# Kernel tuning notes

Hardware: AMD Instinct MI355X
Metric: run time of the kernel (lower is better)

The kernel has to match this reference:

```python
import jax, jax.numpy as jnp
import numpy as np

N = 32768          # nodes
E = 524288         # edges (avg degree 16)
H = 128            # hidden_features
EF = 16            # edge_features
MF = 2 * H + EF + 1  # message_features for e3, relaxed=False (distance feat = 1)


def _mlp2(x, W1, b1, W2, b2):
    # Linear -> silu -> Linear -> silu (edge_mlp)
    return jax.nn.silu(jax.nn.silu(x @ W1 + b1) @ W2 + b2)


def setup_inputs() -> dict:
    key = jax.random.key(0)
    ks = jax.random.split(key, 20)

    def glorot(k, shape):
        fan_in, fan_out = shape[0], shape[1]
        lim = np.sqrt(6.0 / (fan_in + fan_out)).astype(np.float32)
        return jax.random.uniform(k, shape, jnp.float32, -lim, lim)

    inp = {
        'src': jax.random.randint(ks[0], (E,), 0, N),
        'dst': jax.random.randint(ks[1], (E,), 0, N),
        'h': jax.random.normal(ks[2], (N, H), jnp.float32),
        'coords': jax.random.normal(ks[3], (N, 3), jnp.float32),
        'a': jax.random.normal(ks[4], (E, EF), jnp.float32),
        # coord_mlp: MF -> H -> H -> 1 (last bias-free, xavier gain 0.001)
        'W_c1': glorot(ks[5], (MF, H)), 'b_c1': jnp.zeros((H,), jnp.float32),
        'W_c2': glorot(ks[6], (H, H)),  'b_c2': jnp.zeros((H,), jnp.float32),
        'W_c3': glorot(ks[7], (H, 1)) * 0.001,
        # edge_mlp: MF -> H -> H
        'W_e1': glorot(ks[8], (MF, H)), 'b_e1': jnp.zeros((H,), jnp.float32),
        'W_e2': glorot(ks[9], (H, H)),  'b_e2': jnp.zeros((H,), jnp.float32),
        # att_mlp: H -> 1
        'W_att': glorot(ks[10], (H, 1)), 'b_att': jnp.zeros((1,), jnp.float32),
        # node_mlp: 2H -> H -> H
        'W_n1': glorot(ks[11], (2 * H, H)), 'b_n1': jnp.zeros((H,), jnp.float32),
        'W_n2': glorot(ks[12], (H, H)),     'b_n2': jnp.zeros((H,), jnp.float32),
    }
    return inp


def reference(src, dst, h, coords, a,
              W_c1, b_c1, W_c2, b_c2, W_c3,
              W_e1, b_e1, W_e2, b_e2,
              W_att, b_att,
              W_n1, b_n1, W_n2, b_n2):
    # --- edge gather + distance features (equivariance='e3', relaxed=False) ---
    srcs_x = coords[src]                      # [E, 3]
    dsts_x = coords[dst]
    diffs = srcs_x - dsts_x                   # [E, 3]
    radials = jnp.sum(diffs * diffs, axis=-1, keepdims=True)  # [E, 1]

    f = jnp.concatenate([h[src], h[dst], radials, a], axis=-1)  # [E, MF]

    # --- coord messages ---
    c = jax.nn.silu(f @ W_c1 + b_c1)
    c = jax.nn.silu(c @ W_c2 + b_c2)
    scale = c @ W_c3                          # [E, 1]
    msg_x = scale * diffs / (jnp.sqrt(radials + 1e-05) + 1.0)   # [E, 3]

    # --- hidden messages with attention gating ---
    msg_h = _mlp2(f, W_e1, b_e1, W_e2, b_e2)  # [E, H]
    att = jax.nn.sigmoid(msg_h @ W_att + b_att)  # [E, 1]
    msg_h = att * msg_h

    # --- scatter-sum aggregation at destination nodes ---
    x_agg = jax.ops.segment_sum(msg_x, dst, num_segments=N)  # [N, 3]
    h_agg = jax.ops.segment_sum(msg_h, dst, num_segments=N)  # [N, H]

    coords_out = coords + x_agg
    nh = jax.nn.silu(jnp.concatenate([h, h_agg], axis=-1) @ W_n1 + b_n1) @ W_n2 + b_n2
    h_out = h + nh
    return (h_out, coords_out)
```

## Files before the change

### kernel.cpp

```cpp
#include <hip/hip_runtime.h>
#include <math.h>

#define HD   128
#define EFD  16
#define MT   64
#define LPA  264
#define LPC  136

#define W1SZ (128 * 288)
#define W2SZ (128 * 128)
#define O_WE1 (W1SZ)
#define O_WC2 (2 * W1SZ)
#define O_WE2 (2 * W1SZ + W2SZ)
#define O_WN1 (2 * W1SZ + 2 * W2SZ)
#define O_WN2 (2 * W1SZ + 2 * W2SZ + 128 * 256)
#define WS_ELEMS (O_WN2 + W2SZ)

#define B_PSC   ((size_t)0)
#define B_PDC   ((size_t)8388608)
#define B_PSE   ((size_t)16777216)
#define B_PDE   ((size_t)25165824)
#define B_WPAN  ((size_t)33554432)
#define B_CNT   ((size_t)33865728)
#define B_OFS   ((size_t)33996800)
#define B_SRCP  ((size_t)34127872)
#define B_DSTP  ((size_t)36225024)
#define B_EIDX  ((size_t)38322176)

typedef __attribute__((ext_vector_type(8))) short short8;
typedef __attribute__((ext_vector_type(4))) float f32x4;

__device__ __forceinline__ unsigned short f2bf(float x) {
    __bf16 b = (__bf16)x;
    unsigned short u;
    __builtin_memcpy(&u, &b, 2);
    return u;
}
__device__ __forceinline__ float bfl(unsigned u) {
    union { unsigned u; float f; } v; v.u = u << 16; return v.f;
}
__device__ __forceinline__ float bfh(unsigned u) {
    union { unsigned u; float f; } v; v.u = u & 0xffff0000u; return v.f;
}
__device__ __forceinline__ float sigm_f(float x) {
    return __builtin_amdgcn_rcpf(1.f + __expf(-x));
}
__device__ __forceinline__ float silu_f(float x) { return x * sigm_f(x); }
__device__ __forceinline__ unsigned pack2(float a, float b) {
    return (unsigned)f2bf(a) | ((unsigned)f2bf(b) << 16);
}

__device__ __forceinline__ void frag_l1(int idx, const float* __restrict__ W,
                                        const float* __restrict__ bias,
                                        unsigned short* __restrict__ out)
{
    const int j = idx & 7, lane = (idx >> 3) & 63, blk = idx >> 9;
    const int kc = blk % 9, n = blk / 9;
    const int k = kc * 32 + (lane >> 4) * 8 + j;
    const int c = n * 16 + (lane & 15);
    float v = 0.f;
    if (k < 256) v = W[k * HD + c];
    else if (k < 272) v = W[(k + 1) * HD + c];
    else if (k == 272) v = W[256 * HD + c];
    else if (k == 273) v = bias[c];
    out[idx] = f2bf(v);
}
__device__ __forceinline__ void frag_sq(int idx, const float* __restrict__ W,
                                        int nkc, unsigned short* __restrict__ out)
{
    const int j = idx & 7, lane = (idx >> 3) & 63, blk = idx >> 9;
    const int kc = blk % nkc, n = blk / nkc;
    const int k = kc * 32 + (lane >> 4) * 8 + j;
    const int c = n * 16 + (lane & 15);
    out[idx] = f2bf(W[k * HD + c]);
}

__global__ __launch_bounds__(256) void fused_prep(
    const float* __restrict__ Wc1, const float* __restrict__ bc1,
    const float* __restrict__ We1, const float* __restrict__ be1,
    const float* __restrict__ Wc2, const float* __restrict__ We2,
    const float* __restrict__ Wn1, const float* __restrict__ Wn2,
    unsigned short* __restrict__ ws,
    const int* __restrict__ dst, unsigned* __restrict__ cnt,
    int nPrep, int E)
{
    const int bid = blockIdx.x, tid = threadIdx.x;
    if (bid < nPrep) {
        int idx = bid * 256 + tid;
        if (idx < W1SZ)            { frag_l1(idx, Wc1, bc1, ws);            return; }
        idx -= W1SZ;
// ... 68 lines not shown

    #pragma unroll
    for (int it = 0; it < 8; ++it) {
        const int idx = it * 256 + tid;
        const int r = idx >> 5, q = idx & 31;
        const float4 v = *(const float4*)(h + (size_t)(n0 + r) * HD + q * 4);
        uint2 p; p.x = pack2(v.x, v.y); p.y = pack2(v.z, v.w);
        *(uint2*)&hsh[r][q * 4] = p;
    }
    __syncthreads();

    const int lane = tid & 63;
    const int w    = tid >> 6;
    const int w2   = w * 2;
    const int col  = lane & 15;
    const int kg   = lane >> 4;

    pre_pass(wpan + lane * 8,         &hsh[0][0], Psc, Pdc, n0, w2, w, col, kg);
    pre_pass(wpan + O_WE1 + lane * 8, &hsh[0][0], Pse, Pde, n0, w2, w, col, kg);
}

__global__ __launch_bounds__(1024) void scan32k(const unsigned* __restrict__ cnt,
                                                unsigned* __restrict__ ofs)
{
    __shared__ unsigned wsum[16];
    __shared__ unsigned carry_s;
    const int tid = threadIdx.x, lane = tid & 63, w = tid >> 6;
    if (tid == 0) carry_s = 0;
    __syncthreads();
    for (int c = 0; c < 32; ++c) {
        const unsigned x = cnt[c * 1024 + tid];
        unsigned v = x;
        #pragma unroll
        for (int off = 1; off < 64; off <<= 1) {
            unsigned t = __shfl_up(v, off);
            if (lane >= off) v += t;
        }
        if (lane == 63) wsum[w] = v;
        __syncthreads();
        if (tid < 16) {
            unsigned s = wsum[tid];
            #pragma unroll
            for (int off = 1; off < 16; off <<= 1) {
                unsigned t = __shfl_up(s, off);
                if (tid >= off) s += t;
            }
            wsum[tid] = s;
        }
        __syncthreads();
        const unsigned carry = carry_s;
        const unsigned woff = (w == 0) ? 0u : wsum[w - 1];
        ofs[c * 1024 + tid] = carry + woff + v - x;
        __syncthreads();
        if (tid == 0) carry_s = carry + wsum[15];
        __syncthreads();
    }
}

__global__ __launch_bounds__(256) void scatter_perm(
    const int* __restrict__ src, const int* __restrict__ dst,
    unsigned* __restrict__ ofs,
    int* __restrict__ srcp, int* __restrict__ dstp,
    int* __restrict__ eidx, int E)
{
    const int i = blockIdx.x * 256 + threadIdx.x;
    if (i >= E) return;
    const int d = dst[i];
    const unsigned pos = atomicAdd(&ofs[d], 1u);
    srcp[pos] = src[i];
    dstp[pos] = d;
    eidx[pos] = i;
}

__global__ __launch_bounds__(256, 4) void edge_kernel(
    const int* __restrict__ srcp, const int* __restrict__ dstp,
    const int* __restrict__ eidx, const float* __restrict__ a,
    const float* __restrict__ coords,
    const unsigned short* __restrict__ Psc, const unsigned short* __restrict__ Pdc,
    const unsigned short* __restrict__ Pse, const unsigned short* __restrict__ Pde,
    const float* __restrict__ bc2, const float* __restrict__ Wc3,
    const float* __restrict__ be2,
    const float* __restrict__ Watt, const float* __restrict__ batt,
    const unsigned short* __restrict__ wpan,
    float* __restrict__ out_h, float* __restrict__ out_x)
{
    __shared__ __align__(16) unsigned short csh_c[MT][LPC];
    __shared__ __align__(16) unsigned short csh_e[MT][LPC];
    __shared__ float diff_s[MT][3];
    __shared__ float rad_s[MT];
    __shared__ float rinv_s[MT];
    __shared__ float sc_part[4][MT];
    __shared__ float pa_part[4][MT];
    __shared__ float att_s[MT];
    __shared__ float sc_s[MT];
    __shared__ int   src_s[MT], dst_s[MT], eid_s[MT];
    __shared__ short run_start[MT + 1];
    __shared__ int   nruns_s;

    const int tid = threadIdx.x;
    const int e0  = blockIdx.x * MT;

    if (tid < MT) {
        const int s = srcp[e0 + tid], d = dstp[e0 + tid];
        src_s[tid] = s; dst_s[tid] = d;
        eid_s[tid] = eidx[e0 + tid];
        const float dx = coords[(size_t)s*3+0] - coords[(size_t)d*3+0];
        const float dy = coords[(size_t)s*3+1] - coords[(size_t)d*3+1];
        const float dz = coords[(size_t)s*3+2] - coords[(size_t)d*3+2];
        diff_s[tid][0] = dx; diff_s[tid][1] = dy; diff_s[tid][2] = dz;
        const float rad = dx*dx + dy*dy + dz*dz;
        rad_s[tid]  = rad;
        rinv_s[tid] = __builtin_amdgcn_rcpf(sqrtf(rad + 1e-5f) + 1.f);
    }
    __syncthreads();

    if (tid < 64) {
        const bool st = (tid == 0) || (dst_s[tid] != dst_s[tid - 1]);
        unsigned long long m = __ballot(st);
        if (tid == 0) {
            int nr = 0;
            while (m) { run_start[nr++] = (short)__builtin_ctzll(m); m &= m - 1; }
            run_start[nr] = MT;
            nruns_s = nr;
        }
    }

    const int lane = tid & 63;
    const int w    = tid >> 6;
    const int w2   = w * 2;
    const int col  = lane & 15;
    const int kg   = lane >> 4;

    const unsigned short* Wc1p = wpan            + lane * 8;
    const unsigned short* We1p = wpan + O_WE1    + lane * 8;
    const unsigned short* Wc2p = wpan + O_WC2    + lane * 8;
    const unsigned short* We2p = wpan + O_WE2    + lane * 8;

    short8 idf;
    #pragma unroll
    for (int j = 0; j < 8; ++j)
        idf[j] = (short)((((kg * 8 + j) & 15) == col) ? 0x3F80 : 0);

    const unsigned short* bas_c[4];
    const unsigned short* bas_e[4];
    #pragma unroll
    for (int et = 0; et < 4; ++et) {
        const int r = et * 16 + col;
        const size_t so = (size_t)src_s[r] * HD;
        const size_t dofs = (size_t)dst_s[r] * HD;
        const int slot = (kg & 1) * 8;
        bas_c[et] = ((kg < 2) ? Psc + so : Pdc + dofs) + slot;
        bas_e[et] = ((kg < 2) ? Pse + so : Pde + dofs) + slot;
    }

    const short8 zf = {0,0,0,0,0,0,0,0};
    const f32x4 zero = {0.f, 0.f, 0.f, 0.f};
    f32x4 ac[2][4], ae[2][4];

    #pragma unroll
    for (int m = 0; m < 2; ++m)
        #pragma unroll
        for (int et = 0; et < 4; ++et) { ac[m][et] = zero; ae[m][et] = zero; }

    #pragma unroll
    for (int m = 0; m < 2; ++m) {
        const int co = (w2 + m) * 16;
        #pragma unroll
        for (int et = 0; et < 4; ++et) {
            const short8 bc_ = *(const short8*)(bas_c[et] + co);
            const short8 be_ = *(const short8*)(bas_e[et] + co);
            ac[m][et] = __builtin_amdgcn_mfma_f32_16x16x32_bf16(idf, bc_, ac[m][et], 0, 0, 0);
            ae[m][et] = __builtin_amdgcn_mfma_f32_16x16x32_bf16(idf, be_, ae[m][et], 0, 0, 0);
        }
    }
    {
        short8 df[4];
        #pragma unroll
        for (int et = 0; et < 4; ++et) {
            if (kg < 2) {
                const int oe = eid_s[et * 16 + col];
                const float4 a0 = *(const float4*)(a + (size_t)oe * EFD + kg * 8);
                const float4 a1 = *(const float4*)(a + (size_t)oe * EFD + kg * 8 + 4);
                short8 v;
                v[0] = (short)f2bf(a0.x); v[1] = (short)f2bf(a0.y);
                v[2] = (short)f2bf(a0.z); v[3] = (short)f2bf(a0.w);
                v[4] = (short)f2bf(a1.x); v[5] = (short)f2bf(a1.y);
                v[6] = (short)f2bf(a1.z); v[7] = (short)f2bf(a1.w);
                df[et] = v;
            } else if (kg == 2) {
                short8 v = zf;
                v[0] = (short)f2bf(rad_s[et * 16 + col]);
                v[1] = (short)0x3F80;
                df[et] = v;
            } else df[et] = zf;
        }
        #pragma unroll
        for (int m = 0; m < 2; ++m) {
            const short8 wc = *(const short8*)&Wc1p[((w2 + m) * 9 + 8) << 9];
            const short8 we = *(const short8*)&We1p[((w2 + m) * 9 + 8) << 9];
            #pragma unroll
            for (int et = 0; et < 4; ++et) {
                ac[m][et] = __builtin_amdgcn_mfma_f32_16x16x32_bf16(wc, df[et], ac[m][et], 0, 0, 0);
                ae[m][et] = __builtin_amdgcn_mfma_f32_16x16x32_bf16(we, df[et], ae[m][et], 0, 0, 0);
            }
        }
    }
    #pragma unroll
    for (int m = 0; m < 2; ++m)
        #pragma unroll
        for (int et = 0; et < 4; ++et) {
            const int row = et * 16 + col;
            const int hw  = w * 32 + m * 16 + kg * 4;
            uint2 vc, ve;
            vc.x = pack2(silu_f(ac[m][et][0]), silu_f(ac[m][et][1]));
            vc.y = pack2(silu_f(ac[m][et][2]), silu_f(ac[m][et][3]));
            ve.x = pack2(silu_f(ae[m][et][0]), silu_f(ae[m][et][1]));
            ve.y = pack2(silu_f(ae[m][et][2]), silu_f(ae[m][et][3]));
            *(uint2*)&csh_c[row][hw] = vc;
            *(uint2*)&csh_e[row][hw] = ve;
        }
    __syncthreads();

    #pragma unroll
    for (int m = 0; m < 2; ++m)
        #pragma unroll
        for (int et = 0; et < 4; ++et) { ac[m][et] = zero; ae[m][et] = zero; }

    #pragma unroll
    for (int kc = 0; kc < 4; ++kc) {
        short8 dc[4], de[4];
        #pragma unroll
        for (int et = 0; et < 4; ++et) {
            const int row = et * 16 + col;
            dc[et] = *(const short8*)&csh_c[row][kc * 32 + kg * 8];
            de[et] = *(const short8*)&csh_e[row][kc * 32 + kg * 8];
        }
        #pragma unroll
        for (int m = 0; m < 2; ++m) {
            const short8 wc = *(const short8*)&Wc2p[((w2 + m) * 4 + kc) << 9];
            const short8 we = *(const short8*)&We2p[((w2 + m) * 4 + kc) << 9];
            #pragma unroll
            for (int et = 0; et < 4; ++et) {
                ac[m][et] = __builtin_amdgcn_mfma_f32_16x16x32_bf16(wc, dc[et], ac[m][et], 0, 0, 0);
                ae[m][et] = __builtin_amdgcn_mfma_f32_16x16x32_bf16(we, de[et], ae[m][et], 0, 0, 0);
            }
        }
    }

    {
        float sc[4] = {0.f, 0.f, 0.f, 0.f};
        #pragma unroll
        for (int m = 0; m < 2; ++m)
            #pragma unroll
            for (int i = 0; i < 4; ++i) {
                const int hw = w * 32 + m * 16 + kg * 4 + i;
                const float b = bc2[hw], w3 = Wc3[hw];
                #pragma unroll
                for (int et = 0; et < 4; ++et)
                    sc[et] += silu_f(ac[m][et][i] + b) * w3;
            }
        #pragma unroll
        for (int et = 0; et < 4; ++et) {
            sc[et] += __shfl_xor(sc[et], 16);
            sc[et] += __shfl_xor(sc[et], 32);
        }
        if (kg == 0) {
            #pragma unroll
            for (int et = 0; et < 4; ++et)
                sc_part[w][et * 16 + col] = sc[et];
        }
    }
    __syncthreads();

    {
        float pa[4] = {0.f, 0.f, 0.f, 0.f};
        #pragma unroll
        for (int m = 0; m < 2; ++m)
            #pragma unroll
            for (int et = 0; et < 4; ++et) {
                const int row = et * 16 + col;
                const int hw  = w * 32 + m * 16 + kg * 4;
                const float v0 = silu_f(ae[m][et][0] + be2[hw]);
                const float v1 = silu_f(ae[m][et][1] + be2[hw+1]);
                const float v2 = silu_f(ae[m][et][2] + be2[hw+2]);
                const float v3 = silu_f(ae[m][et][3] + be2[hw+3]);
                pa[et] += v0 * Watt[hw] + v1 * Watt[hw+1]
                        + v2 * Watt[hw+2] + v3 * Watt[hw+3];
                uint2 ve;
                ve.x = pack2(v0, v1);
                ve.y = pack2(v2, v3);
                *(uint2*)&csh_e[row][hw] = ve;
            }
        #pragma unroll
        for (int et = 0; et < 4; ++et) {
            pa[et] += __shfl_xor(pa[et], 16);
            pa[et] += __shfl_xor(pa[et], 32);
        }
        if (kg == 0) {
            #pragma unroll
            for (int et = 0; et < 4; ++et)
                pa_part[w][et * 16 + col] = pa[et];
        }
    }
    __syncthreads();

    if (tid < MT) {
        att_s[tid] = sigm_f(pa_part[0][tid] + pa_part[1][tid] +
                            pa_part[2][tid] + pa_part[3][tid] + batt[0]);
        sc_s[tid]  = (sc_part[0][tid] + sc_part[1][tid] +
                      sc_part[2][tid] + sc_part[3][tid]) * rinv_s[tid];
    }
    __syncthreads();

    {
        const int nr    = nruns_s;
        const int colx2 = tid & 63;
        for (int r = tid >> 6; r < nr; r += 4) {
            const int s0 = run_start[r], s1 = run_start[r + 1];
            float sum0 = 0.f, sum1 = 0.f;
            for (int e = s0; e < s1; ++e) {
                const unsigned uv = *(const unsigned*)&csh_e[e][colx2 * 2];
                const float at = att_s[e];
                sum0 += bfl(uv) * at;
                sum1 += bfh(uv) * at;
            }
            const int drow = dst_s[s0];
            float* op = out_h + (size_t)drow * HD + colx2 * 2;
            atomicAdd(op,     sum0);
            atomicAdd(op + 1, sum1);
            if (colx2 < 2) {
                float sx0 = 0.f, sx1 = 0.f;
                for (int e = s0; e < s1; ++e) {
                    const float s = sc_s[e];
                    sx0 += s * diff_s[e][colx2 * 2];
                    if (colx2 == 0) sx1 += s * diff_s[e][1];
                }
                atomicAdd(&out_x[(size_t)drow * 3 + colx2 * 2], sx0);
                if (colx2 == 0) atomicAdd(&out_x[(size_t)drow * 3 + 1], sx1);
            }
        }
    }
}

__global__ __launch_bounds__(256) void node_kernel(
    const float* __restrict__ h, const float* __restrict__ coords,
    const float* __restrict__ bn1, const float* __restrict__ bn2,
    const unsigned short* __restrict__ wpan,
    float* __restrict__ out_h, float* __restrict__ out_x)
{
    __shared__ __align__(16) unsigned short ash[MT][LPA];
    __shared__ __align__(16) unsigned short csh[MT][LPC];

    const int tid = threadIdx.x;
    const int n0  = blockIdx.x * MT;

    #pragma unroll
    for (int it = 0; it < 16; ++it) {
        const int idx = it * 256 + tid;
        const int e = idx >> 6, q = idx & 63;
        const float* base = (q < 32)
            ? h     + (size_t)(n0 + e) * HD + q * 4
            : out_h + (size_t)(n0 + e) * HD + (q - 32) * 4;
        const float4 v = *(const float4*)base;
        uint2 p; p.x = pack2(v.x, v.y); p.y = pack2(v.z, v.w);
        *(uint2*)&ash[e][q * 4] = p;
    }
    __syncthreads();

    if (tid < MT * 3) {
        const int n = tid / 3, d = tid % 3;
        const size_t gi = (size_t)(n0 + n) * 3 + d;
        out_x[gi] += coords[gi];
    }

    const int lane = tid & 63;
    const int w    = tid >> 6;
    const int er0  = w * 16;
    const int col  = lane & 15;
    const int kg   = lane >> 4;

    const unsigned short* Wn1p = wpan + O_WN1 + lane * 8;
    const unsigned short* Wn2p = wpan + O_WN2 + lane * 8;

    const f32x4 zero = {0.f, 0.f, 0.f, 0.f};
    f32x4 acc[8];

    #pragma unroll
    for (int n = 0; n < 8; ++n) acc[n] = zero;
    #pragma unroll
    for (int kc = 0; kc < 8; ++kc) {
        const short8 af = *(const short8*)&ash[er0 + col][kc * 32 + kg * 8];
        #pragma unroll
        for (int n = 0; n < 8; ++n) {
            const short8 bf = *(const short8*)&Wn1p[(n * 8 + kc) << 9];
            acc[n] = __builtin_amdgcn_mfma_f32_16x16x32_bf16(af, bf, acc[n], 0, 0, 0);
        }
    }
    #pragma unroll
    for (int n = 0; n < 8; ++n) {
        const float b = bn1[n*16 + col];
        #pragma unroll
        for (int i = 0; i < 4; ++i)
            csh[er0 + kg*4 + i][n*16 + col] = f2bf(silu_f(acc[n][i] + b));
    }
    __syncthreads();
    #pragma unroll
    for (int n = 0; n < 8; ++n) acc[n] = zero;
    #pragma unroll
    for (int kc = 0; kc < 4; ++kc) {
        const short8 af = *(const short8*)&csh[er0 + col][kc * 32 + kg * 8];
        #pragma unroll
        for (int n = 0; n < 8; ++n) {
            const short8 bf = *(const short8*)&Wn2p[(n * 4 + kc) << 9];
            acc[n] = __builtin_amdgcn_mfma_f32_16x16x32_bf16(af, bf, acc[n], 0, 0, 0);
        }
    }
    #pragma unroll
    for (int i = 0; i < 4; ++i) {
        const int node = n0 + er0 + kg*4 + i;
        const float* hr   = h     + (size_t)node * HD;
        float*       orow = out_h + (size_t)node * HD;
        #pragma unroll
        for (int n = 0; n < 8; ++n) {
            const int f = n*16 + col;
            orow[f] = hr[f] + acc[n][i] + bn2[f];
        }
    }
}

extern "C" void kernel_launch(void* const* d_in, const int* in_sizes, int n_in,
                              void* d_out, int out_size, void* d_ws, size_t ws_size,
                              hipStream_t stream)
{
    const int*   src    = (const int*)  d_in[0];
    const int*   dst    = (const int*)  d_in[1];
    const float* h      = (const float*)d_in[2];
    const float* coords = (const float*)d_in[3];
    const float* a      = (const float*)d_in[4];
    const float* Wc1    = (const float*)d_in[5];
    const float* bc1    = (const float*)d_in[6];
    const float* Wc2    = (const float*)d_in[7];
    const float* bc2    = (const float*)d_in[8];
    const float* Wc3    = (const float*)d_in[9];
    const float* We1    = (const float*)d_in[10];
    const float* be1    = (const float*)d_in[11];
    const float* We2    = (const float*)d_in[12];
    const float* be2    = (const float*)d_in[13];
    const float* Watt   = (const float*)d_in[14];
    const float* batt   = (const float*)d_in[15];
    const float* Wn1    = (const float*)d_in[16];
    const float* bn1    = (const float*)d_in[17];
    const float* Wn2    = (const float*)d_in[18];
    const float* bn2    = (const float*)d_in[19];

    const int E = in_sizes[0];
    const int N = in_sizes[2] / HD;

    float* out_h = (float*)d_out;
    float* out_x = out_h + (size_t)N * HD;

    char* wsb = (char*)d_ws;
    unsigned short* Psc  = (unsigned short*)(wsb + B_PSC);
    unsigned short* Pdc  = (unsigned short*)(wsb + B_PDC);
    unsigned short* Pse  = (unsigned short*)(wsb + B_PSE);
    unsigned short* Pde  = (unsigned short*)(wsb + B_PDE);
    unsigned short* wpan = (unsigned short*)(wsb + B_WPAN);
    unsigned*       cnt  = (unsigned*)      (wsb + B_CNT);
    unsigned*       ofs  = (unsigned*)      (wsb + B_OFS);
    int*            srcp = (int*)           (wsb + B_SRCP);
    int*            dstp = (int*)           (wsb + B_DSTP);
    int*            eidx = (int*)           (wsb + B_EIDX);

    hipMemsetAsync(d_out, 0, (size_t)out_size * sizeof(float), stream);
    hipMemsetAsync(cnt, 0, (size_t)N * sizeof(unsigned), stream);

    const int nPrep = WS_ELEMS / 256;
    const int nHist = (E + 255) / 256;

    fused_prep<<<dim3(nPrep + nHist), dim3(256), 0, stream>>>(
        Wc1, bc1, We1, be1, Wc2, We2, Wn1, Wn2, wpan,
        dst, cnt, nPrep, E);

    node_pre<<<dim3(N / MT), dim3(256), 0, stream>>>(
        h, wpan, Psc, Pdc, Pse, Pde);

    scan32k<<<dim3(1), dim3(1024), 0, stream>>>(cnt, ofs);
    scatter_perm<<<dim3((E + 255) / 256), dim3(256), 0, stream>>>(
        src, dst, ofs, srcp, dstp, eidx, E);

    edge_kernel<<<dim3(E / MT), dim3(256), 0, stream>>>(
        srcp, dstp, eidx, a, coords,
        Psc, Pdc, Pse, Pde,
        bc2, Wc3, be2, Watt, batt,
        wpan, out_h, out_x);

    node_kernel<<<dim3(N / MT), dim3(256), 0, stream>>>(
        h, coords, bn1, bn2, wpan, out_h, out_x);
}
```

Before: 312.0 us.

## Make edge kernel persistent with software-prefetched gathers for the next tile

The edge kernel now launches 1024 blocks that each loop over several 64-edge tiles instead of one block per tile. Index loads, the precomputed-projection gathers, edge-id loads and coordinate reads for the next tile are issued into registers and double-buffered shared arrays while the current tile finishes its MLP and scatter. The goal is to hide gather latency behind compute and cut per-block launch and setup cost. In exchange the kernel holds more live registers, which can lower occupancy, and runs fewer blocks.

```diff
diff --git a/kernel.cpp b/kernel.cpp
--- a/kernel.cpp
+++ b/kernel.cpp
@@ -240,7 +240,7 @@
     const float* __restrict__ be2,
     const float* __restrict__ Watt, const float* __restrict__ batt,
     const unsigned short* __restrict__ wpan,
-    float* __restrict__ out_h, float* __restrict__ out_x)
+    float* __restrict__ out_h, float* __restrict__ out_x, int ntPer)
 {
     __shared__ __align__(16) unsigned short csh_c[MT][LPC];
     __shared__ __align__(16) unsigned short csh_e[MT][LPC];
@@ -251,43 +251,17 @@
     __shared__ float pa_part[4][MT];
     __shared__ float att_s[MT];
     __shared__ float sc_s[MT];
-    __shared__ int   src_s[MT], dst_s[MT], eid_s[MT];
-    __shared__ short run_start[MT + 1];
+    __shared__ int   src_s[2][MT], dst_s[2][MT];
+    __shared__ short run_start[MT + 2];
     __shared__ int   nruns_s;
 
-    const int tid = threadIdx.x;
-    const int e0  = blockIdx.x * MT;
-
-    if (tid < MT) {
-        const int s = srcp[e0 + tid], d = dstp[e0 + tid];
-        src_s[tid] = s; dst_s[tid] = d;
-        eid_s[tid] = eidx[e0 + tid];
-        const float dx = coords[(size_t)s*3+0] - coords[(size_t)d*3+0];
-        const float dy = coords[(size_t)s*3+1] - coords[(size_t)d*3+1];
-        const float dz = coords[(size_t)s*3+2] - coords[(size_t)d*3+2];
-        diff_s[tid][0] = dx; diff_s[tid][1] = dy; diff_s[tid][2] = dz;
-        const float rad = dx*dx + dy*dy + dz*dz;
-        rad_s[tid]  = rad;
-        rinv_s[tid] = __builtin_amdgcn_rcpf(sqrtf(rad + 1e-5f) + 1.f);
-    }
-    __syncthreads();
-
-    if (tid < 64) {
-        const bool st = (tid == 0) || (dst_s[tid] != dst_s[tid - 1]);
-        unsigned long long m = __ballot(st);
-        if (tid == 0) {
-            int nr = 0;
-            while (m) { run_start[nr++] = (short)__builtin_ctzll(m); m &= m - 1; }
-            run_start[nr] = MT;
-            nruns_s = nr;
-        }
-    }
-
+    const int tid  = threadIdx.x;
     const int lane = tid & 63;
     const int w    = tid >> 6;
     const int w2   = w * 2;
     const int col  = lane & 15;
     const int kg   = lane >> 4;
+    const int tile0 = blockIdx.x * ntPer;
 
     const unsigned short* Wc1p = wpan            + lane * 8;
     const unsigned short* We1p = wpan + O_WE1    + lane * 8;
@@ -299,202 +273,258 @@
     for (int j = 0; j < 8; ++j)
         idf[j] = (short)((((kg * 8 + j) & 15) == col) ? 0x3F80 : 0);
 
-    const unsigned short* bas_c[4];
-    const unsigned short* bas_e[4];
-    #pragma unroll
-    for (int et = 0; et < 4; ++et) {
-        const int r = et * 16 + col;
-        const size_t so = (size_t)src_s[r] * HD;
-        const size_t dofs = (size_t)dst_s[r] * HD;
-        const int slot = (kg & 1) * 8;
-        bas_c[et] = ((kg < 2) ? Psc + so : Pdc + dofs) + slot;
-        bas_e[et] = ((kg < 2) ? Pse + so : Pde + dofs) + slot;
-    }
-
     const short8 zf = {0,0,0,0,0,0,0,0};
     const f32x4 zero = {0.f, 0.f, 0.f, 0.f};
-    f32x4 ac[2][4], ae[2][4];
-
-    #pragma unroll
-    for (int m = 0; m < 2; ++m)
-        #pragma unroll
-        for (int et = 0; et < 4; ++et) { ac[m][et] = zero; ae[m][et] = zero; }
-
-    #pragma unroll
-    for (int m = 0; m < 2; ++m) {
-        const int co = (w2 + m) * 16;
+
+    short8 pfc[2][4], pfe[2][4];
+    int    eidn[4];
+    float  cxs[3], cxd[3];
+
+    auto issue_gathers = [&](int buf, int e1) {
         #pragma unroll
         for (int et = 0; et < 4; ++et) {
-            const short8 bc_ = *(const short8*)(bas_c[et] + co);
-            const short8 be_ = *(const short8*)(bas_e[et] + co);
-            ac[m][et] = __builtin_amdgcn_mfma_f32_16x16x32_bf16(idf, bc_, ac[m][et], 0, 0, 0);
-            ae[m][et] = __builtin_amdgcn_mfma_f32_16x16x32_bf16(idf, be_, ae[m][et], 0, 0, 0);
-        }
-    }
+            const int r = et * 16 + col;
+            const size_t so   = (size_t)src_s[buf][r] * HD;
+            const size_t dofs = (size_t)dst_s[buf][r] * HD;
+            const int slot = (kg & 1) * 8;
+            const unsigned short* bc = ((kg < 2) ? Psc + so : Pdc + dofs) + slot;
+            const unsigned short* be = ((kg < 2) ? Pse + so : Pde + dofs) + slot;
+            pfc[0][et] = *(const short8*)(bc + w2 * 16);
+            pfc[1][et] = *(const short8*)(bc + (w2 + 1) * 16);
+            pfe[0][et] = *(const short8*)(be + w2 * 16);
+            pfe[1][et] = *(const short8*)(be + (w2 + 1) * 16);
+            eidn[et] = eidx[e1 + r];
+        }
+    };
+    auto issue_coords = [&](int buf) {
+        if (tid < MT) {
+            const int s = src_s[buf][tid], d = dst_s[buf][tid];
+            cxs[0] = coords[(size_t)s*3+0]; cxs[1] = coords[(size_t)s*3+1]; cxs[2] = coords[(size_t)s*3+2];
+            cxd[0] = coords[(size_t)d*3+0]; cxd[1] = coords[(size_t)d*3+1]; cxd[2] = coords[(size_t)d*3+2];
+        }
+    };
+
     {
-        short8 df[4];
-        #pragma unroll
-        for (int et = 0; et < 4; ++et) {
-            if (kg < 2) {
-                const int oe = eid_s[et * 16 + col];
-                const float4 a0 = *(const float4*)(a + (size_t)oe * EFD + kg * 8);
-                const float4 a1 = *(const float4*)(a + (size_t)oe * EFD + kg * 8 + 4);
-                short8 v;
-                v[0] = (short)f2bf(a0.x); v[1] = (short)f2bf(a0.y);
-                v[2] = (short)f2bf(a0.z); v[3] = (short)f2bf(a0.w);
-                v[4] = (short)f2bf(a1.x); v[5] = (short)f2bf(a1.y);
-                v[6] = (short)f2bf(a1.z); v[7] = (short)f2bf(a1.w);
-                df[et] = v;
-            } else if (kg == 2) {
-                short8 v = zf;
-                v[0] = (short)f2bf(rad_s[et * 16 + col]);
-                v[1] = (short)0x3F80;
-                df[et] = v;
-            } else df[et] = zf;
-        }
-        #pragma unroll
-        for (int m = 0; m < 2; ++m) {
-            const short8 wc = *(const short8*)&Wc1p[((w2 + m) * 9 + 8) << 9];
-            const short8 we = *(const short8*)&We1p[((w2 + m) * 9 + 8) << 9];
+        const int e1 = tile0 * MT;
+        if (tid < MT) {
+            src_s[0][tid] = srcp[e1 + tid];
+            dst_s[0][tid] = dstp[e1 + tid];
+        }
+        __syncthreads();
+        issue_gathers(0, e1);
+        issue_coords(0);
+    }
+
+    for (int t = 0; t < ntPer; ++t) {
+        const int cur = t & 1, nxt = cur ^ 1;
+        const int e0  = (tile0 + t) * MT;
+        const bool more = (t + 1 < ntPer);
+
+        __syncthreads();
+
+        if (tid < MT) {
+            const float dx = cxs[0] - cxd[0];
+            const float dy = cxs[1] - cxd[1];
+            const float dz = cxs[2] - cxd[2];
+            diff_s[tid][0] = dx; diff_s[tid][1] = dy; diff_s[tid][2] = dz;
+            const float rad = dx*dx + dy*dy + dz*dz;
+            rad_s[tid]  = rad;
+            rinv_s[tid] = __builtin_amdgcn_rcpf(sqrtf(rad + 1e-5f) + 1.f);
+            const bool st = (tid == 0) || (dst_s[cur][tid] != dst_s[cur][tid - 1]);
+            unsigned long long m = __ballot(st);
+            if (tid == 0) {
+                int nr = 0;
+                while (m) { run_start[nr++] = (short)__builtin_ctzll(m); m &= m - 1; }
+                run_start[nr] = MT;
+                nruns_s = nr;
+            }
+        }
+        __syncthreads();
+
+        f32x4 ac[2][4], ae[2][4];
+
+        #pragma unroll
+        for (int m = 0; m < 2; ++m)
             #pragma unroll
             for (int et = 0; et < 4; ++et) {
-                ac[m][et] = __builtin_amdgcn_mfma_f32_16x16x32_bf16(wc, df[et], ac[m][et], 0, 0, 0);
-                ae[m][et] = __builtin_amdgcn_mfma_f32_16x16x32_bf16(we, df[et], ae[m][et], 0, 0, 0);
-            }
-        }
-    }
-    #pragma unroll
-    for (int m = 0; m < 2; ++m)
-        #pragma unroll
-        for (int et = 0; et < 4; ++et) {
-            const int row = et * 16 + col;
-            const int hw  = w * 32 + m * 16 + kg * 4;
-            uint2 vc, ve;
-            vc.x = pack2(silu_f(ac[m][et][0]), silu_f(ac[m][et][1]));
-            vc.y = pack2(silu_f(ac[m][et][2]), silu_f(ac[m][et][3]));
-            ve.x = pack2(silu_f(ae[m][et][0]), silu_f(ae[m][et][1]));
-            ve.y = pack2(silu_f(ae[m][et][2]), silu_f(ae[m][et][3]));
-            *(uint2*)&csh_c[row][hw] = vc;
-            *(uint2*)&csh_e[row][hw] = ve;
-        }
-    __syncthreads();
-
-    #pragma unroll
-    for (int m = 0; m < 2; ++m)
-        #pragma unroll
-        for (int et = 0; et < 4; ++et) { ac[m][et] = zero; ae[m][et] = zero; }
-
-    #pragma unroll
-    for (int kc = 0; kc < 4; ++kc) {
-        short8 dc[4], de[4];
-        #pragma unroll
-        for (int et = 0; et < 4; ++et) {
-            const int row = et * 16 + col;
-            dc[et] = *(const short8*)&csh_c[row][kc * 32 + kg * 8];
-            de[et] = *(const short8*)&csh_e[row][kc * 32 + kg * 8];
-        }
-        #pragma unroll
-        for (int m = 0; m < 2; ++m) {
-            const short8 wc = *(const short8*)&Wc2p[((w2 + m) * 4 + kc) << 9];
-            const short8 we = *(const short8*)&We2p[((w2 + m) * 4 + kc) << 9];
+                ac[m][et] = __builtin_amdgcn_mfma_f32_16x16x32_bf16(idf, pfc[m][et], zero, 0, 0, 0);
+                ae[m][et] = __builtin_amdgcn_mfma_f32_16x16x32_bf16(idf, pfe[m][et], zero, 0, 0, 0);
+            }
+        {
+            short8 df[4];
             #pragma unroll
             for (int et = 0; et < 4; ++et) {
-                ac[m][et] = __builtin_amdgcn_mfma_f32_16x16x32_bf16(wc, dc[et], ac[m][et], 0, 0, 0);
-                ae[m][et] = __builtin_amdgcn_mfma_f32_16x16x32_bf16(we, de[et], ae[m][et], 0, 0, 0);
-            }
-        }
-    }
-
-    {
-        float sc[4] = {0.f, 0.f, 0.f, 0.f};
-        #pragma unroll
-        for (int m = 0; m < 2; ++m)
-            #pragma unroll
-            for (int i = 0; i < 4; ++i) {
-                const int hw = w * 32 + m * 16 + kg * 4 + i;
-                const float b = bc2[hw], w3 = Wc3[hw];
+                if (kg < 2) {
+                    const int oe = eidn[et];
+                    const float4 a0 = *(const float4*)(a + (size_t)oe * EFD + kg * 8);
+                    const float4 a1 = *(const float4*)(a + (size_t)oe * EFD + kg * 8 + 4);
+                    short8 v;
+                    v[0] = (short)f2bf(a0.x); v[1] = (short)f2bf(a0.y);
+                    v[2] = (short)f2bf(a0.z); v[3] = (short)f2bf(a0.w);
+                    v[4] = (short)f2bf(a1.x); v[5] = (short)f2bf(a1.y);
+                    v[6] = (short)f2bf(a1.z); v[7] = (short)f2bf(a1.w);
+                    df[et] = v;
+                } else if (kg == 2) {
+                    short8 v = zf;
+                    v[0] = (short)f2bf(rad_s[et * 16 + col]);
+                    v[1] = (short)0x3F80;
+                    df[et] = v;
+                } else df[et] = zf;
+            }
+            #pragma unroll
+            for (int m = 0; m < 2; ++m) {
+                const short8 wc = *(const short8*)&Wc1p[((w2 + m) * 9 + 8) << 9];
+                const short8 we = *(const short8*)&We1p[((w2 + m) * 9 + 8) << 9];
                 #pragma unroll
-                for (int et = 0; et < 4; ++et)
-                    sc[et] += silu_f(ac[m][et][i] + b) * w3;
-            }
-        #pragma unroll
-        for (int et = 0; et < 4; ++et) {
-            sc[et] += __shfl_xor(sc[et], 16);
-            sc[et] += __shfl_xor(sc[et], 32);
-        }
-        if (kg == 0) {
-            #pragma unroll
-            for (int et = 0; et < 4; ++et)
-                sc_part[w][et * 16 + col] = sc[et];
-        }
-    }
-    __syncthreads();
-
-    {
-        float pa[4] = {0.f, 0.f, 0.f, 0.f};
+                for (int et = 0; et < 4; ++et) {
+                    ac[m][et] = __builtin_amdgcn_mfma_f32_16x16x32_bf16(wc, df[et], ac[m][et], 0, 0, 0);
+                    ae[m][et] = __builtin_amdgcn_mfma_f32_16x16x32_bf16(we, df[et], ae[m][et], 0, 0, 0);
+                }
+            }
+        }
         #pragma unroll
         for (int m = 0; m < 2; ++m)
             #pragma unroll
             for (int et = 0; et < 4; ++et) {
                 const int row = et * 16 + col;
                 const int hw  = w * 32 + m * 16 + kg * 4;
-                const float v0 = silu_f(ae[m][et][0] + be2[hw]);
-                const float v1 = silu_f(ae[m][et][1] + be2[hw+1]);
-                const float v2 = silu_f(ae[m][et][2] + be2[hw+2]);
-                const float v3 = silu_f(ae[m][et][3] + be2[hw+3]);
-                pa[et] += v0 * Watt[hw] + v1 * Watt[hw+1]
-                        + v2 * Watt[hw+2] + v3 * Watt[hw+3];
-                uint2 ve;
-                ve.x = pack2(v0, v1);
-                ve.y = pack2(v2, v3);
+                uint2 vc, ve;
+                vc.x = pack2(silu_f(ac[m][et][0]), silu_f(ac[m][et][1]));
+                vc.y = pack2(silu_f(ac[m][et][2]), silu_f(ac[m][et][3]));
+                ve.x = pack2(silu_f(ae[m][et][0]), silu_f(ae[m][et][1]));
+                ve.y = pack2(silu_f(ae[m][et][2]), silu_f(ae[m][et][3]));
+                *(uint2*)&csh_c[row][hw] = vc;
                 *(uint2*)&csh_e[row][hw] = ve;
             }
-        #pragma unroll
-        for (int et = 0; et < 4; ++et) {
-            pa[et] += __shfl_xor(pa[et], 16);
-            pa[et] += __shfl_xor(pa[et], 32);
-        }
-        if (kg == 0) {
-            #pragma unroll
-            for (int et = 0; et < 4; ++et)
-                pa_part[w][et * 16 + col] = pa[et];
-        }
-    }
-    __syncthreads();
-
-    if (tid < MT) {
-        att_s[tid] = sigm_f(pa_part[0][tid] + pa_part[1][tid] +
-                            pa_part[2][tid] + pa_part[3][tid] + batt[0]);
-        sc_s[tid]  = (sc_part[0][tid] + sc_part[1][tid] +
-                      sc_part[2][tid] + sc_part[3][tid]) * rinv_s[tid];
-    }
-    __syncthreads();
-
-    {
-        const int nr    = nruns_s;
-        const int colx2 = tid & 63;
-        for (int r = tid >> 6; r < nr; r += 4) {
-            const int s0 = run_start[r], s1 = run_start[r + 1];
-            float sum0 = 0.f, sum1 = 0.f;
-            for (int e = s0; e < s1; ++e) {
-                const unsigned uv = *(const unsigned*)&csh_e[e][colx2 * 2];
-                const float at = att_s[e];
-                sum0 += bfl(uv) * at;
-                sum1 += bfh(uv) * at;
-            }
-            const int drow = dst_s[s0];
-            float* op = out_h + (size_t)drow * HD + colx2 * 2;
-            atomicAdd(op,     sum0);
-            atomicAdd(op + 1, sum1);
-            if (colx2 < 2) {
-                float sx0 = 0.f, sx1 = 0.f;
+        if (more && tid < MT) {
+            const int e1 = e0 + MT;
+            src_s[nxt][tid] = srcp[e1 + tid];
+            dst_s[nxt][tid] = dstp[e1 + tid];
+        }
+        __syncthreads();
+
+        #pragma unroll
+        for (int m = 0; m < 2; ++m)
+            #pragma unroll
+            for (int et = 0; et < 4; ++et) { ac[m][et] = zero; ae[m][et] = zero; }
+
+        #pragma unroll
+        for (int kc = 0; kc < 4; ++kc) {
+            short8 dc[4], de[4];
+            #pragma unroll
+            for (int et = 0; et < 4; ++et) {
+                const int row = et * 16 + col;
+                dc[et] = *(const short8*)&csh_c[row][kc * 32 + kg * 8];
+                de[et] = *(const short8*)&csh_e[row][kc * 32 + kg * 8];
+            }
+            #pragma unroll
+            for (int m = 0; m < 2; ++m) {
+                const short8 wc = *(const short8*)&Wc2p[((w2 + m) * 4 + kc) << 9];
+                const short8 we = *(const short8*)&We2p[((w2 + m) * 4 + kc) << 9];
+                #pragma unroll
+                for (int et = 0; et < 4; ++et) {
+                    ac[m][et] = __builtin_amdgcn_mfma_f32_16x16x32_bf16(wc, dc[et], ac[m][et], 0, 0, 0);
+                    ae[m][et] = __builtin_amdgcn_mfma_f32_16x16x32_bf16(we, de[et], ae[m][et], 0, 0, 0);
+                }
+            }
+        }
+
+        {
+            float sc[4] = {0.f, 0.f, 0.f, 0.f};
+            #pragma unroll
+            for (int m = 0; m < 2; ++m)
+                #pragma unroll
+                for (int i = 0; i < 4; ++i) {
+                    const int hw = w * 32 + m * 16 + kg * 4 + i;
+                    const float b = bc2[hw], w3 = Wc3[hw];
+                    #pragma unroll
+                    for (int et = 0; et < 4; ++et)
+                        sc[et] += silu_f(ac[m][et][i] + b) * w3;
+                }
+            #pragma unroll
+            for (int et = 0; et < 4; ++et) {
+                sc[et] += __shfl_xor(sc[et], 16);
+                sc[et] += __shfl_xor(sc[et], 32);
+            }
+            if (kg == 0) {
+                #pragma unroll
+                for (int et = 0; et < 4; ++et)
+                    sc_part[w][et * 16 + col] = sc[et];
+            }
+        }
+        __syncthreads();
+
+        {
+            float pa[4] = {0.f, 0.f, 0.f, 0.f};
+            #pragma unroll
+            for (int m = 0; m < 2; ++m)
+                #pragma unroll
+                for (int et = 0; et < 4; ++et) {
+                    const int row = et * 16 + col;
+                    const int hw  = w * 32 + m * 16 + kg * 4;
+                    const float v0 = silu_f(ae[m][et][0] + be2[hw]);
+                    const float v1 = silu_f(ae[m][et][1] + be2[hw+1]);
+                    const float v2 = silu_f(ae[m][et][2] + be2[hw+2]);
+                    const float v3 = silu_f(ae[m][et][3] + be2[hw+3]);
+                    pa[et] += v0 * Watt[hw] + v1 * Watt[hw+1]
+                            + v2 * Watt[hw+2] + v3 * Watt[hw+3];
+                    uint2 ve;
+                    ve.x = pack2(v0, v1);
+                    ve.y = pack2(v2, v3);
+                    *(uint2*)&csh_e[row][hw] = ve;
+                }
+            #pragma unroll
+            for (int et = 0; et < 4; ++et) {
+                pa[et] += __shfl_xor(pa[et], 16);
+                pa[et] += __shfl_xor(pa[et], 32);
+            }
+            if (kg == 0) {
+                #pragma unroll
+                for (int et = 0; et < 4; ++et)
+                    pa_part[w][et * 16 + col] = pa[et];
+            }
+        }
+        __syncthreads();
+
+        if (tid < MT) {
+            att_s[tid] = sigm_f(pa_part[0][tid] + pa_part[1][tid] +
+                                pa_part[2][tid] + pa_part[3][tid] + batt[0]);
+            sc_s[tid]  = (sc_part[0][tid] + sc_part[1][tid] +
+                          sc_part[2][tid] + sc_part[3][tid]) * rinv_s[tid];
+        }
+
+        if (more) {
+            issue_gathers(nxt, e0 + MT);
+            issue_coords(nxt);
+        }
+        __syncthreads();
+
+        {
+            const int nr    = nruns_s;
+            const int colx2 = tid & 63;
+            for (int r = tid >> 6; r < nr; r += 4) {
+                const int s0 = run_start[r], s1 = run_start[r + 1];
+                float sum0 = 0.f, sum1 = 0.f;
                 for (int e = s0; e < s1; ++e) {
-                    const float s = sc_s[e];
-                    sx0 += s * diff_s[e][colx2 * 2];
-                    if (colx2 == 0) sx1 += s * diff_s[e][1];
+                    const unsigned uv = *(const unsigned*)&csh_e[e][colx2 * 2];
+                    const float at = att_s[e];
+                    sum0 += bfl(uv) * at;
+                    sum1 += bfh(uv) * at;
                 }
-                atomicAdd(&out_x[(size_t)drow * 3 + colx2 * 2], sx0);
-                if (colx2 == 0) atomicAdd(&out_x[(size_t)drow * 3 + 1], sx1);
+                const int drow = dst_s[cur][s0];
+                float* op = out_h + (size_t)drow * HD + colx2 * 2;
+                atomicAdd(op,     sum0);
+                atomicAdd(op + 1, sum1);
+                if (colx2 < 2) {
+                    float sx0 = 0.f, sx1 = 0.f;
+                    for (int e = s0; e < s1; ++e) {
+                        const float s = sc_s[e];
+                        sx0 += s * diff_s[e][colx2 * 2];
+                        if (colx2 == 0) sx1 += s * diff_s[e][1];
+                    }
+                    atomicAdd(&out_x[(size_t)drow * 3 + colx2 * 2], sx0);
+                    if (colx2 == 0) atomicAdd(&out_x[(size_t)drow * 3 + 1], sx1);
+                }
             }
         }
     }
@@ -646,11 +676,15 @@
     scatter_perm<<<dim3((E + 255) / 256), dim3(256), 0, stream>>>(
         src, dst, ofs, srcp, dstp, eidx, E);
 
-    edge_kernel<<<dim3(E / MT), dim3(256), 0, stream>>>(
+    const int ntiles = E / MT;
+    int nblk = 1024, ntPer = ntiles / 1024;
+    if (ntiles % 1024) { nblk = ntiles; ntPer = 1; }
+
+    edge_kernel<<<dim3(nblk), dim3(256), 0, stream>>>(
         srcp, dstp, eidx, a, coords,
         Psc, Pdc, Pse, Pde,
         bc2, Wc3, be2, Watt, batt,
-        wpan, out_h, out_x);
+        wpan, out_h, out_x, ntPer);
 
     node_kernel<<<dim3(N / MT), dim3(256), 0, stream>>>(
         h, coords, bn1, bn2, wpan, out_h, out_x);
```

Result: slower. 766.6 us (+145.7%).

## Make edge kernel wave-independent with per-wave 16-edge tiles and no block barriers

Applied to the files above, without the earlier changes.

Restructures the edge kernel so each wave handles its own 16 edges end to end instead of four waves cooperating on a 64-edge tile split by output columns. Shared-memory staging, partial-sum tables and __syncthreads are replaced by per-wave LDS slices, wave barriers and shuffles for edge metadata, attention and scale values. This removes block-wide synchronisation and cross-wave reductions. In exchange, segment runs are shorter, so more atomics are issued per destination, and each wave now reads all of the layer weights itself.

```diff
diff --git a/kernel.cpp b/kernel.cpp
--- a/kernel.cpp
+++ b/kernel.cpp
@@ -4,8 +4,10 @@
 #define HD   128
 #define EFD  16
 #define MT   64
+#define WT   16
 #define LPA  264
 #define LPC  136
+#define LPW  132
 
 #define W1SZ (128 * 288)
 #define W2SZ (128 * 128)
@@ -242,52 +244,42 @@
     const unsigned short* __restrict__ wpan,
     float* __restrict__ out_h, float* __restrict__ out_x)
 {
-    __shared__ __align__(16) unsigned short csh_c[MT][LPC];
-    __shared__ __align__(16) unsigned short csh_e[MT][LPC];
-    __shared__ float diff_s[MT][3];
-    __shared__ float rad_s[MT];
-    __shared__ float rinv_s[MT];
-    __shared__ float sc_part[4][MT];
-    __shared__ float pa_part[4][MT];
-    __shared__ float att_s[MT];
-    __shared__ float sc_s[MT];
-    __shared__ int   src_s[MT], dst_s[MT], eid_s[MT];
-    __shared__ short run_start[MT + 1];
-    __shared__ int   nruns_s;
-
-    const int tid = threadIdx.x;
-    const int e0  = blockIdx.x * MT;
-
-    if (tid < MT) {
-        const int s = srcp[e0 + tid], d = dstp[e0 + tid];
-        src_s[tid] = s; dst_s[tid] = d;
-        eid_s[tid] = eidx[e0 + tid];
-        const float dx = coords[(size_t)s*3+0] - coords[(size_t)d*3+0];
-        const float dy = coords[(size_t)s*3+1] - coords[(size_t)d*3+1];
-        const float dz = coords[(size_t)s*3+2] - coords[(size_t)d*3+2];
-        diff_s[tid][0] = dx; diff_s[tid][1] = dy; diff_s[tid][2] = dz;
-        const float rad = dx*dx + dy*dy + dz*dz;
-        rad_s[tid]  = rad;
-        rinv_s[tid] = __builtin_amdgcn_rcpf(sqrtf(rad + 1e-5f) + 1.f);
-    }
-    __syncthreads();
-
-    if (tid < 64) {
-        const bool st = (tid == 0) || (dst_s[tid] != dst_s[tid - 1]);
-        unsigned long long m = __ballot(st);
-        if (tid == 0) {
-            int nr = 0;
-            while (m) { run_start[nr++] = (short)__builtin_ctzll(m); m &= m - 1; }
-            run_start[nr] = MT;
-            nruns_s = nr;
-        }
-    }
-
+    __shared__ __align__(16) unsigned short csh_c[4][WT][LPW];
+    __shared__ __align__(16) unsigned short csh_e[4][WT][LPW];
+
+    const int tid  = threadIdx.x;
     const int lane = tid & 63;
     const int w    = tid >> 6;
-    const int w2   = w * 2;
     const int col  = lane & 15;
     const int kg   = lane >> 4;
+    const int e0   = (blockIdx.x * 4 + w) * WT;
+
+    int srcv = 0, dstv = 0, eidv = 0;
+    float dfx = 0.f, dfy = 0.f, dfz = 0.f, radv = 0.f, rinvv = 0.f;
+    if (lane < WT) {
+        srcv = srcp[e0 + lane];
+        dstv = dstp[e0 + lane];
+        eidv = eidx[e0 + lane];
+        const float sx = coords[(size_t)srcv*3+0], sy = coords[(size_t)srcv*3+1], sz = coords[(size_t)srcv*3+2];
+        const float dx_ = coords[(size_t)dstv*3+0], dy_ = coords[(size_t)dstv*3+1], dz_ = coords[(size_t)dstv*3+2];
+        dfx = sx - dx_; dfy = sy - dy_; dfz = sz - dz_;
+        radv = dfx*dfx + dfy*dfy + dfz*dfz;
+        rinvv = __builtin_amdgcn_rcpf(sqrtf(radv + 1e-5f) + 1.f);
+    }
+    const int   se    = __shfl(srcv, col);
+    const int   de_   = __shfl(dstv, col);
+    const int   ee    = __shfl(eidv, col);
+    const float rad_c = __shfl(radv, col);
+
+    const int prevd = __shfl_up(dstv, 1);
+    const bool st = (lane < WT) && (lane == 0 || dstv != prevd);
+    const unsigned long long mask = __ballot(st) & 0xffffull;
+
+    const size_t so   = (size_t)se  * HD;
+    const size_t dofs = (size_t)de_ * HD;
+    const int slot = (kg & 1) * 8;
+    const unsigned short* bas_c = ((kg < 2) ? Psc + so : Pdc + dofs) + slot;
+    const unsigned short* bas_e = ((kg < 2) ? Pse + so : Pde + dofs) + slot;
 
     const unsigned short* Wc1p = wpan            + lane * 8;
     const unsigned short* We1p = wpan + O_WE1    + lane * 8;
@@ -299,202 +291,118 @@
     for (int j = 0; j < 8; ++j)
         idf[j] = (short)((((kg * 8 + j) & 15) == col) ? 0x3F80 : 0);
 
-    const unsigned short* bas_c[4];
-    const unsigned short* bas_e[4];
-    #pragma unroll
-    for (int et = 0; et < 4; ++et) {
-        const int r = et * 16 + col;
-        const size_t so = (size_t)src_s[r] * HD;
-        const size_t dofs = (size_t)dst_s[r] * HD;
-        const int slot = (kg & 1) * 8;
-        bas_c[et] = ((kg < 2) ? Psc + so : Pdc + dofs) + slot;
-        bas_e[et] = ((kg < 2) ? Pse + so : Pde + dofs) + slot;
-    }
-
     const short8 zf = {0,0,0,0,0,0,0,0};
     const f32x4 zero = {0.f, 0.f, 0.f, 0.f};
-    f32x4 ac[2][4], ae[2][4];
-
-    #pragma unroll
-    for (int m = 0; m < 2; ++m)
-        #pragma unroll
-        for (int et = 0; et < 4; ++et) { ac[m][et] = zero; ae[m][et] = zero; }
-
-    #pragma unroll
-    for (int m = 0; m < 2; ++m) {
-        const int co = (w2 + m) * 16;
-        #pragma unroll
-        for (int et = 0; et < 4; ++et) {
-            const short8 bc_ = *(const short8*)(bas_c[et] + co);
-            const short8 be_ = *(const short8*)(bas_e[et] + co);
-            ac[m][et] = __builtin_amdgcn_mfma_f32_16x16x32_bf16(idf, bc_, ac[m][et], 0, 0, 0);
-            ae[m][et] = __builtin_amdgcn_mfma_f32_16x16x32_bf16(idf, be_, ae[m][et], 0, 0, 0);
-        }
-    }
+
+    short8 df;
+    if (kg < 2) {
+        const float4 a0 = *(const float4*)(a + (size_t)ee * EFD + kg * 8);
+        const float4 a1 = *(const float4*)(a + (size_t)ee * EFD + kg * 8 + 4);
+        df[0] = (short)f2bf(a0.x); df[1] = (short)f2bf(a0.y);
+        df[2] = (short)f2bf(a0.z); df[3] = (short)f2bf(a0.w);
+        df[4] = (short)f2bf(a1.x); df[5] = (short)f2bf(a1.y);
+        df[6] = (short)f2bf(a1.z); df[7] = (short)f2bf(a1.w);
+    } else if (kg == 2) {
+        df = zf;
+        df[0] = (short)f2bf(rad_c);
+        df[1] = (short)0x3F80;
+    } else df = zf;
+
+    #pragma unroll
+    for (int m = 0; m < 8; ++m) {
+        const short8 bc_ = *(const short8*)(bas_c + m * 16);
+        const short8 be_ = *(const short8*)(bas_e + m * 16);
+        f32x4 ac = __builtin_amdgcn_mfma_f32_16x16x32_bf16(idf, bc_, zero, 0, 0, 0);
+        f32x4 ae = __builtin_amdgcn_mfma_f32_16x16x32_bf16(idf, be_, zero, 0, 0, 0);
+        const short8 wc = *(const short8*)&Wc1p[(m * 9 + 8) << 9];
+        const short8 we = *(const short8*)&We1p[(m * 9 + 8) << 9];
+        ac = __builtin_amdgcn_mfma_f32_16x16x32_bf16(wc, df, ac, 0, 0, 0);
+        ae = __builtin_amdgcn_mfma_f32_16x16x32_bf16(we, df, ae, 0, 0, 0);
+        const int hw = m * 16 + kg * 4;
+        uint2 vc, ve;
+        vc.x = pack2(silu_f(ac[0]), silu_f(ac[1]));
+        vc.y = pack2(silu_f(ac[2]), silu_f(ac[3]));
+        ve.x = pack2(silu_f(ae[0]), silu_f(ae[1]));
+        ve.y = pack2(silu_f(ae[2]), silu_f(ae[3]));
+        *(uint2*)&csh_c[w][col][hw] = vc;
+        *(uint2*)&csh_e[w][col][hw] = ve;
+    }
+    __builtin_amdgcn_wave_barrier();
+
+    short8 dc[4], de2[4];
+    #pragma unroll
+    for (int kc = 0; kc < 4; ++kc) {
+        dc[kc]  = *(const short8*)&csh_c[w][col][kc * 32 + kg * 8];
+        de2[kc] = *(const short8*)&csh_e[w][col][kc * 32 + kg * 8];
+    }
+    __builtin_amdgcn_wave_barrier();
+
+    float scl = 0.f, pal = 0.f;
+    #pragma unroll
+    for (int m = 0; m < 8; ++m) {
+        f32x4 ac = zero, ae = zero;
+        #pragma unroll
+        for (int kc = 0; kc < 4; ++kc) {
+            const short8 wc = *(const short8*)&Wc2p[(m * 4 + kc) << 9];
+            const short8 we = *(const short8*)&We2p[(m * 4 + kc) << 9];
+            ac = __builtin_amdgcn_mfma_f32_16x16x32_bf16(wc, dc[kc],  ac, 0, 0, 0);
+            ae = __builtin_amdgcn_mfma_f32_16x16x32_bf16(we, de2[kc], ae, 0, 0, 0);
+        }
+        const int hw = m * 16 + kg * 4;
+        const float4 b2 = *(const float4*)(bc2 + hw);
+        const float4 w3 = *(const float4*)(Wc3 + hw);
+        scl += silu_f(ac[0] + b2.x) * w3.x + silu_f(ac[1] + b2.y) * w3.y
+             + silu_f(ac[2] + b2.z) * w3.z + silu_f(ac[3] + b2.w) * w3.w;
+        const float4 be_ = *(const float4*)(be2 + hw);
+        const float4 wa  = *(const float4*)(Watt + hw);
+        const float v0 = silu_f(ae[0] + be_.x);
+        const float v1 = silu_f(ae[1] + be_.y);
+        const float v2 = silu_f(ae[2] + be_.z);
+        const float v3 = silu_f(ae[3] + be_.w);
+        pal += v0 * wa.x + v1 * wa.y + v2 * wa.z + v3 * wa.w;
+        uint2 ve;
+        ve.x = pack2(v0, v1);
+        ve.y = pack2(v2, v3);
+        *(uint2*)&csh_e[w][col][hw] = ve;
+    }
+    __builtin_amdgcn_wave_barrier();
+
+    scl += __shfl_xor(scl, 16);
+    scl += __shfl_xor(scl, 32);
+    pal += __shfl_xor(pal, 16);
+    pal += __shfl_xor(pal, 32);
+    const float att_v = sigm_f(pal + batt[0]);
+    const float sc_v  = scl * __shfl(rinvv, col);
+
     {
-        short8 df[4];
-        #pragma unroll
-        for (int et = 0; et < 4; ++et) {
-            if (kg < 2) {
-                const int oe = eid_s[et * 16 + col];
-                const float4 a0 = *(const float4*)(a + (size_t)oe * EFD + kg * 8);
-                const float4 a1 = *(const float4*)(a + (size_t)oe * EFD + kg * 8 + 4);
-                short8 v;
-                v[0] = (short)f2bf(a0.x); v[1] = (short)f2bf(a0.y);
-                v[2] = (short)f2bf(a0.z); v[3] = (short)f2bf(a0.w);
-                v[4] = (short)f2bf(a1.x); v[5] = (short)f2bf(a1.y);
-                v[6] = (short)f2bf(a1.z); v[7] = (short)f2bf(a1.w);
-                df[et] = v;
-            } else if (kg == 2) {
-                short8 v = zf;
-                v[0] = (short)f2bf(rad_s[et * 16 + col]);
-                v[1] = (short)0x3F80;
-                df[et] = v;
-            } else df[et] = zf;
-        }
-        #pragma unroll
-        for (int m = 0; m < 2; ++m) {
-            const short8 wc = *(const short8*)&Wc1p[((w2 + m) * 9 + 8) << 9];
-            const short8 we = *(const short8*)&We1p[((w2 + m) * 9 + 8) << 9];
-            #pragma unroll
-            for (int et = 0; et < 4; ++et) {
-                ac[m][et] = __builtin_amdgcn_mfma_f32_16x16x32_bf16(wc, df[et], ac[m][et], 0, 0, 0);
-                ae[m][et] = __builtin_amdgcn_mfma_f32_16x16x32_bf16(we, df[et], ae[m][et], 0, 0, 0);
-            }
-        }
-    }
-    #pragma unroll
-    for (int m = 0; m < 2; ++m)
-        #pragma unroll
-        for (int et = 0; et < 4; ++et) {
-            const int row = et * 16 + col;
-            const int hw  = w * 32 + m * 16 + kg * 4;
-            uint2 vc, ve;
-            vc.x = pack2(silu_f(ac[m][et][0]), silu_f(ac[m][et][1]));
-            vc.y = pack2(silu_f(ac[m][et][2]), silu_f(ac[m][et][3]));
-            ve.x = pack2(silu_f(ae[m][et][0]), silu_f(ae[m][et][1]));
-            ve.y = pack2(silu_f(ae[m][et][2]), silu_f(ae[m][et][3]));
-            *(uint2*)&csh_c[row][hw] = vc;
-            *(uint2*)&csh_e[row][hw] = ve;
-        }
-    __syncthreads();
-
-    #pragma unroll
-    for (int m = 0; m < 2; ++m)
-        #pragma unroll
-        for (int et = 0; et < 4; ++et) { ac[m][et] = zero; ae[m][et] = zero; }
-
-    #pragma unroll
-    for (int kc = 0; kc < 4; ++kc) {
-        short8 dc[4], de[4];
-        #pragma unroll
-        for (int et = 0; et < 4; ++et) {
-            const int row = et * 16 + col;
-            dc[et] = *(const short8*)&csh_c[row][kc * 32 + kg * 8];
-            de[et] = *(const short8*)&csh_e[row][kc * 32 + kg * 8];
-        }
-        #pragma unroll
-        for (int m = 0; m < 2; ++m) {
-            const short8 wc = *(const short8*)&Wc2p[((w2 + m) * 4 + kc) << 9];
-            const short8 we = *(const short8*)&We2p[((w2 + m) * 4 + kc) << 9];
-            #pragma unroll
-            for (int et = 0; et < 4; ++et) {
-                ac[m][et] = __builtin_amdgcn_mfma_f32_16x16x32_bf16(wc, dc[et], ac[m][et], 0, 0, 0);
-                ae[m][et] = __builtin_amdgcn_mfma_f32_16x16x32_bf16(we, de[et], ae[m][et], 0, 0, 0);
-            }
-        }
-    }
-
-    {
-        float sc[4] = {0.f, 0.f, 0.f, 0.f};
-        #pragma unroll
-        for (int m = 0; m < 2; ++m)
-            #pragma unroll
-            for (int i = 0; i < 4; ++i) {
-                const int hw = w * 32 + m * 16 + kg * 4 + i;
-                const float b = bc2[hw], w3 = Wc3[hw];
-                #pragma unroll
-                for (int et = 0; et < 4; ++et)
-                    sc[et] += silu_f(ac[m][et][i] + b) * w3;
-            }
-        #pragma unroll
-        for (int et = 0; et < 4; ++et) {
-            sc[et] += __shfl_xor(sc[et], 16);
-            sc[et] += __shfl_xor(sc[et], 32);
-        }
-        if (kg == 0) {
-            #pragma unroll
-            for (int et = 0; et < 4; ++et)
-                sc_part[w][et * 16 + col] = sc[et];
-        }
-    }
-    __syncthreads();
-
-    {
-        float pa[4] = {0.f, 0.f, 0.f, 0.f};
-        #pragma unroll
-        for (int m = 0; m < 2; ++m)
-            #pragma unroll
-            for (int et = 0; et < 4; ++et) {
-                const int row = et * 16 + col;
-                const int hw  = w * 32 + m * 16 + kg * 4;
-                const float v0 = silu_f(ae[m][et][0] + be2[hw]);
-                const float v1 = silu_f(ae[m][et][1] + be2[hw+1]);
-                const float v2 = silu_f(ae[m][et][2] + be2[hw+2]);
-                const float v3 = silu_f(ae[m][et][3] + be2[hw+3]);
-                pa[et] += v0 * Watt[hw] + v1 * Watt[hw+1]
-                        + v2 * Watt[hw+2] + v3 * Watt[hw+3];
-                uint2 ve;
-                ve.x = pack2(v0, v1);
-                ve.y = pack2(v2, v3);
-                *(uint2*)&csh_e[row][hw] = ve;
-            }
-        #pragma unroll
-        for (int et = 0; et < 4; ++et) {
-            pa[et] += __shfl_xor(pa[et], 16);
-            pa[et] += __shfl_xor(pa[et], 32);
-        }
-        if (kg == 0) {
-            #pragma unroll
-            for (int et = 0; et < 4; ++et)
-                pa_part[w][et * 16 + col] = pa[et];
-        }
-    }
-    __syncthreads();
-
-    if (tid < MT) {
-        att_s[tid] = sigm_f(pa_part[0][tid] + pa_part[1][tid] +
-                            pa_part[2][tid] + pa_part[3][tid] + batt[0]);
-        sc_s[tid]  = (sc_part[0][tid] + sc_part[1][tid] +
-                      sc_part[2][tid] + sc_part[3][tid]) * rinv_s[tid];
-    }
-    __syncthreads();
-
-    {
-        const int nr    = nruns_s;
-        const int colx2 = tid & 63;
-        for (int r = tid >> 6; r < nr; r += 4) {
-            const int s0 = run_start[r], s1 = run_start[r + 1];
-            float sum0 = 0.f, sum1 = 0.f;
+        unsigned long long mm = mask;
+        while (mm) {
+            const int s0 = (int)__builtin_ctzll(mm);
+            mm &= mm - 1;
+            const int s1 = mm ? (int)__builtin_ctzll(mm) : WT;
+            float sum0 = 0.f, sum1 = 0.f, sx0 = 0.f, sx1 = 0.f;
             for (int e = s0; e < s1; ++e) {
-                const unsigned uv = *(const unsigned*)&csh_e[e][colx2 * 2];
-                const float at = att_s[e];
+                const unsigned uv = *(const unsigned*)&csh_e[w][e][lane * 2];
+                const float at = __shfl(att_v, e);
                 sum0 += bfl(uv) * at;
                 sum1 += bfh(uv) * at;
+                const float sce = __shfl(sc_v, e);
+                const float d0 = __shfl(dfx, e);
+                const float d1 = __shfl(dfy, e);
+                const float d2 = __shfl(dfz, e);
+                if (lane == 0) { sx0 += sce * d0; sx1 += sce * d1; }
+                if (lane == 1) { sx0 += sce * d2; }
             }
-            const int drow = dst_s[s0];
-            float* op = out_h + (size_t)drow * HD + colx2 * 2;
+            const int drow = __shfl(dstv, s0);
+            float* op = out_h + (size_t)drow * HD + lane * 2;
             atomicAdd(op,     sum0);
             atomicAdd(op + 1, sum1);
-            if (colx2 < 2) {
-                float sx0 = 0.f, sx1 = 0.f;
-                for (int e = s0; e < s1; ++e) {
-                    const float s = sc_s[e];
-                    sx0 += s * diff_s[e][colx2 * 2];
-                    if (colx2 == 0) sx1 += s * diff_s[e][1];
-                }
-                atomicAdd(&out_x[(size_t)drow * 3 + colx2 * 2], sx0);
-                if (colx2 == 0) atomicAdd(&out_x[(size_t)drow * 3 + 1], sx1);
+            if (lane == 0) {
+                atomicAdd(&out_x[(size_t)drow * 3 + 0], sx0);
+                atomicAdd(&out_x[(size_t)drow * 3 + 1], sx1);
+            }
+            if (lane == 1) {
+                atomicAdd(&out_x[(size_t)drow * 3 + 2], sx0);
             }
         }
     }
@@ -646,7 +554,7 @@
     scatter_perm<<<dim3((E + 255) / 256), dim3(256), 0, stream>>>(
         src, dst, ofs, srcp, dstp, eidx, E);
 
-    edge_kernel<<<dim3(E / MT), dim3(256), 0, stream>>>(
+    edge_kernel<<<dim3(E / (4 * WT)), dim3(256), 0, stream>>>(
         srcp, dstp, eidx, a, coords,
         Psc, Pdc, Pse, Pde,
         bc2, Wc3, be2, Watt, batt,
```

Result: slower. 352.4 us (+13.0%).
